# Kernel optimization log

Hardware: AMD Instinct MI355X
Metric: run time of the kernel (lower is better)

Reference implementation:

```python
import jax, jax.numpy as jnp
import numpy as np

TWO_PI = 6.283185307179586
B, D, NC = 2097152, 8, 1024


def _apply_rot(s0, s1, phi, theta, omega):
    """Apply PennyLane Rot(phi, theta, omega) = RZ(omega) RY(theta) RZ(phi)
    to a batch of single-qubit states (s0, s1). All angle args float32."""
    c = jnp.cos(theta * 0.5)
    s = jnp.sin(theta * 0.5)
    u00 = jnp.exp(-0.5j * (phi + omega)) * c
    u01 = -jnp.exp(0.5j * (phi - omega)) * s
    u10 = jnp.exp(-0.5j * (phi - omega)) * s
    u11 = jnp.exp(0.5j * (phi + omega)) * c
    return u00 * s0 + u01 * s1, u10 * s0 + u11 * s1


def setup_inputs() -> dict:
    key = jax.random.key(0)
    k1, k2, k3 = jax.random.split(key, 3)
    instance = jax.random.uniform(k1, (B, D, 3), dtype=jnp.float32) * TWO_PI
    concept_index = jax.random.randint(k2, (B, D), 0, NC, dtype=jnp.int64)
    # product concept -> init uniform in [0, 2*pi)
    concept_weights = jax.random.uniform(k3, (NC, 3), dtype=jnp.float32) * TWO_PI
    return {"instance": instance, "concept_index": concept_index,
            "concept_weights": concept_weights}


def reference(instance, concept_index, concept_weights):
    # embedding gather: [B, D, 3]
    concept = concept_weights[concept_index]
    # per-domain single-qubit circuit: |0> -> Rot(instance) -> Rot(concept)
    s0 = jnp.ones((B, D), dtype=jnp.complex64)
    s1 = jnp.zeros((B, D), dtype=jnp.complex64)
    s0, s1 = _apply_rot(s0, s1, instance[..., 0], instance[..., 1], instance[..., 2])
    s0, s1 = _apply_rot(s0, s1, concept[..., 0], concept[..., 1], concept[..., 2])
    # expval(PauliZ) per wire, then map to probability as in forward()
    z = (s0.real * s0.real + s0.imag * s0.imag) - (s1.real * s1.real + s1.imag * s1.imag)
    return z * 0.5 + 0.5  # [batch, domain]
```

## Files before the change

kernel.cpp:

```cpp
#include <hip/hip_runtime.h>
#include <math.h>

#define NCONCEPT 1024


__global__ __launch_bounds__(256) void vqc_kernel(
    const float* __restrict__ inst,
    const int*   __restrict__ idx,
    const float* __restrict__ w,
    float*       __restrict__ out,
    int n)
{
    __shared__ float4 tab[NCONCEPT];

    for (int c = threadIdx.x; c < NCONCEPT; c += blockDim.x) {
        float ph2 = w[c * 3 + 0];
        float th2 = w[c * 3 + 1];
        float sth2, cth2, sph2, cph2;
        __sincosf(th2, &sth2, &cth2);
        __sincosf(ph2, &sph2, &cph2);
        tab[c] = make_float4(cth2, sth2, cph2, sph2);
    }
    __syncthreads();

    const int tid    = blockIdx.x * blockDim.x + threadIdx.x;
    const int stride = gridDim.x * blockDim.x;
    const int nquads = n >> 2;

    const float4* __restrict__ inst4 = (const float4*)inst;
    const int4*   __restrict__ idx4  = (const int4*)idx;
    float4*       __restrict__ out4  = (float4*)out;

    for (int q = tid; q < nquads; q += stride) {
        float4 a = inst4[q * 3 + 0];
        float4 b = inst4[q * 3 + 1];
        float4 c = inst4[q * 3 + 2];
        int4   ix = idx4[q];

        float th[4] = { a.y, b.x, b.w, c.z };
        float om[4] = { a.z, b.y, c.x, c.w };
        int   id[4] = { ix.x, ix.y, ix.z, ix.w };

        float res[4];
        #pragma unroll
        for (int e = 0; e < 4; ++e) {
            float4 t = tab[id[e]];
            float s1, c1, so, co;
            __sincosf(th[e], &s1, &c1);
            __sincosf(om[e], &so, &co);
            float cop = co * t.z - so * t.w;
            float z   = t.x * c1 - t.y * s1 * cop;
            res[e] = fmaf(z, 0.5f, 0.5f);
        }
        out4[q] = make_float4(res[0], res[1], res[2], res[3]);
    }

    for (int i = (nquads << 2) + tid; i < n; i += stride) {
        float th1 = inst[i * 3 + 1];
        float om1 = inst[i * 3 + 2];
        float4 t = tab[idx[i]];
        float s1, c1, so, co;
        __sincosf(th1, &s1, &c1);
        __sincosf(om1, &so, &co);
        float cop = co * t.z - so * t.w;
        float z   = t.x * c1 - t.y * s1 * cop;
        out[i] = fmaf(z, 0.5f, 0.5f);
    }
}

extern "C" void kernel_launch(void* const* d_in, const int* in_sizes, int n_in,
                              void* d_out, int out_size, void* d_ws, size_t ws_size,
                              hipStream_t stream) {
    const float* inst = (const float*)d_in[0];
    const int*   idx  = (const int*)d_in[1];
    const float* w    = (const float*)d_in[2];
    float*       out  = (float*)d_out;

    const int n = in_sizes[1];
    const int blocks = 2048;
    vqc_kernel<<<blocks, 256, 0, stream>>>(inst, idx, w, out, n);
}
```

Baseline: 64.54 us.

## Process eight elements per thread with nontemporal loads and a split LUT

Each thread now handles eight elements per iteration, issuing six 16-byte instance loads and two index loads, all nontemporal, plus nontemporal output stores. The shared concept table is split into a cos array and a premultiplied (sin*cos, sin*sin) float2 array. This removes per-element multiplies and shrinks LDS reads from 16 to 12 bytes. The larger unroll adds more loads in flight per thread but raises register pressure.

```diff
diff --git a/kernel.cpp b/kernel.cpp
--- a/kernel.cpp
+++ b/kernel.cpp
@@ -2,6 +2,10 @@
 #include <math.h>
 
 #define NCONCEPT 1024
+
+typedef float fx4 __attribute__((ext_vector_type(4)));
+typedef int   ix4 __attribute__((ext_vector_type(4)));
+typedef float fx2 __attribute__((ext_vector_type(2)));
 
 
 __global__ __launch_bounds__(256) void vqc_kernel(
@@ -11,7 +15,8 @@
     float*       __restrict__ out,
     int n)
 {
-    __shared__ float4 tab[NCONCEPT];
+    __shared__ float tabA[NCONCEPT];
+    __shared__ fx2   tabB[NCONCEPT];
 
     for (int c = threadIdx.x; c < NCONCEPT; c += blockDim.x) {
         float ph2 = w[c * 3 + 0];
@@ -19,51 +24,62 @@
         float sth2, cth2, sph2, cph2;
         __sincosf(th2, &sth2, &cth2);
         __sincosf(ph2, &sph2, &cph2);
-        tab[c] = make_float4(cth2, sth2, cph2, sph2);
+        tabA[c] = cth2;
+        fx2 b; b.x = sth2 * cph2; b.y = sth2 * sph2;
+        tabB[c] = b;
     }
     __syncthreads();
 
     const int tid    = blockIdx.x * blockDim.x + threadIdx.x;
     const int stride = gridDim.x * blockDim.x;
-    const int nquads = n >> 2;
+    const int nocts  = n >> 3;
 
-    const float4* __restrict__ inst4 = (const float4*)inst;
-    const int4*   __restrict__ idx4  = (const int4*)idx;
-    float4*       __restrict__ out4  = (float4*)out;
+    const fx4* __restrict__ inst4 = (const fx4*)inst;
+    const ix4* __restrict__ idx4  = (const ix4*)idx;
+    fx4*       __restrict__ out4  = (fx4*)out;
 
-    for (int q = tid; q < nquads; q += stride) {
-        float4 a = inst4[q * 3 + 0];
-        float4 b = inst4[q * 3 + 1];
-        float4 c = inst4[q * 3 + 2];
-        int4   ix = idx4[q];
+    for (int q = tid; q < nocts; q += stride) {
+        fx4 a0 = __builtin_nontemporal_load(&inst4[q * 6 + 0]);
+        fx4 a1 = __builtin_nontemporal_load(&inst4[q * 6 + 1]);
+        fx4 a2 = __builtin_nontemporal_load(&inst4[q * 6 + 2]);
+        fx4 a3 = __builtin_nontemporal_load(&inst4[q * 6 + 3]);
+        fx4 a4 = __builtin_nontemporal_load(&inst4[q * 6 + 4]);
+        fx4 a5 = __builtin_nontemporal_load(&inst4[q * 6 + 5]);
+        ix4 i0 = __builtin_nontemporal_load(&idx4[q * 2 + 0]);
+        ix4 i1 = __builtin_nontemporal_load(&idx4[q * 2 + 1]);
 
-        float th[4] = { a.y, b.x, b.w, c.z };
-        float om[4] = { a.z, b.y, c.x, c.w };
-        int   id[4] = { ix.x, ix.y, ix.z, ix.w };
+        float th[8] = { a0.y, a1.x, a1.w, a2.z, a3.y, a4.x, a4.w, a5.z };
+        float om[8] = { a0.z, a1.y, a2.x, a2.w, a3.z, a4.y, a5.x, a5.w };
+        int   id[8] = { i0.x, i0.y, i0.z, i0.w, i1.x, i1.y, i1.z, i1.w };
 
-        float res[4];
+        float res[8];
         #pragma unroll
-        for (int e = 0; e < 4; ++e) {
-            float4 t = tab[id[e]];
+        for (int e = 0; e < 8; ++e) {
+            float A  = tabA[id[e]];
+            fx2   Bv = tabB[id[e]];
             float s1, c1, so, co;
             __sincosf(th[e], &s1, &c1);
             __sincosf(om[e], &so, &co);
-            float cop = co * t.z - so * t.w;
-            float z   = t.x * c1 - t.y * s1 * cop;
+            float cop = Bv.x * co - Bv.y * so;
+            float z   = A * c1 - s1 * cop;
             res[e] = fmaf(z, 0.5f, 0.5f);
         }
-        out4[q] = make_float4(res[0], res[1], res[2], res[3]);
+        fx4 r0, r1;
+        r0.x = res[0]; r0.y = res[1]; r0.z = res[2]; r0.w = res[3];
+        r1.x = res[4]; r1.y = res[5]; r1.z = res[6]; r1.w = res[7];
+        __builtin_nontemporal_store(r0, &out4[q * 2 + 0]);
+        __builtin_nontemporal_store(r1, &out4[q * 2 + 1]);
     }
 
-    for (int i = (nquads << 2) + tid; i < n; i += stride) {
+    for (int i = (nocts << 3) + tid; i < n; i += stride) {
         float th1 = inst[i * 3 + 1];
         float om1 = inst[i * 3 + 2];
-        float4 t = tab[idx[i]];
+        float A   = tabA[idx[i]];
+        fx2   Bv  = tabB[idx[i]];
         float s1, c1, so, co;
         __sincosf(th1, &s1, &c1);
         __sincosf(om1, &so, &co);
-        float cop = co * t.z - so * t.w;
-        float z   = t.x * c1 - t.y * s1 * cop;
+        float z = A * c1 - s1 * (Bv.x * co - Bv.y * so);
         out[i] = fmaf(z, 0.5f, 0.5f);
     }
 }
```

Result: slower. 111.9 us (+73.3%).

## Switch to per-element strided loads with 4-way unrolled batching and prefolded table

Applied to the files above, without the earlier changes.

Replaces the per-thread quad processing, which used three float4 instance loads and one int4 index load, with per-element accesses. Each thread now issues four independent element loads across grid strides, reading only theta and omega as an unaligned float2, so the unused phi is never requested. The concept table now stores cos(theta), sin(theta)cos(phi) and sin(theta)sin(phi) precomputed, saving a multiply per element. The cost is narrower, stride-3 gathers in place of wide vector loads, which may reduce coalescing efficiency, though cache lines are still fully fetched.

```diff
diff --git a/kernel.cpp b/kernel.cpp
--- a/kernel.cpp
+++ b/kernel.cpp
@@ -2,68 +2,65 @@
 #include <math.h>
 
 #define NCONCEPT 1024
+#define TPB 256
+#define UNROLL 4
+
+typedef float fx4  __attribute__((ext_vector_type(4)));
+typedef float fx2u __attribute__((ext_vector_type(2), aligned(4)));
 
 
-__global__ __launch_bounds__(256) void vqc_kernel(
+__global__ __launch_bounds__(TPB) void vqc_kernel(
     const float* __restrict__ inst,
     const int*   __restrict__ idx,
     const float* __restrict__ w,
     float*       __restrict__ out,
     int n)
 {
-    __shared__ float4 tab[NCONCEPT];
+    __shared__ fx4 tab[NCONCEPT];
 
-    for (int c = threadIdx.x; c < NCONCEPT; c += blockDim.x) {
+    for (int c = threadIdx.x; c < NCONCEPT; c += TPB) {
         float ph2 = w[c * 3 + 0];
         float th2 = w[c * 3 + 1];
         float sth2, cth2, sph2, cph2;
         __sincosf(th2, &sth2, &cth2);
         __sincosf(ph2, &sph2, &cph2);
-        tab[c] = make_float4(cth2, sth2, cph2, sph2);
+        fx4 t; t.x = cth2; t.y = sth2 * cph2; t.z = sth2 * sph2; t.w = 0.0f;
+        tab[c] = t;
     }
     __syncthreads();
 
-    const int tid    = blockIdx.x * blockDim.x + threadIdx.x;
-    const int stride = gridDim.x * blockDim.x;
-    const int nquads = n >> 2;
+    const int tid = blockIdx.x * TPB + threadIdx.x;
+    const int T   = gridDim.x * TPB;
 
-    const float4* __restrict__ inst4 = (const float4*)inst;
-    const int4*   __restrict__ idx4  = (const int4*)idx;
-    float4*       __restrict__ out4  = (float4*)out;
-
-    for (int q = tid; q < nquads; q += stride) {
-        float4 a = inst4[q * 3 + 0];
-        float4 b = inst4[q * 3 + 1];
-        float4 c = inst4[q * 3 + 2];
-        int4   ix = idx4[q];
-
-        float th[4] = { a.y, b.x, b.w, c.z };
-        float om[4] = { a.z, b.y, c.x, c.w };
-        int   id[4] = { ix.x, ix.y, ix.z, ix.w };
-
-        float res[4];
+    int i = tid;
+    for (; i + (UNROLL - 1) * T < n; i += UNROLL * T) {
+        fx2u to_[UNROLL];
+        int  id_[UNROLL];
         #pragma unroll
-        for (int e = 0; e < 4; ++e) {
-            float4 t = tab[id[e]];
+        for (int u = 0; u < UNROLL; ++u) {
+            const int e = i + u * T;
+            to_[u] = *(const fx2u*)(inst + (size_t)e * 3 + 1);
+            id_[u] = idx[e];
+        }
+        #pragma unroll
+        for (int u = 0; u < UNROLL; ++u) {
+            const int e = i + u * T;
+            fx4 t4 = tab[id_[u]];
             float s1, c1, so, co;
-            __sincosf(th[e], &s1, &c1);
-            __sincosf(om[e], &so, &co);
-            float cop = co * t.z - so * t.w;
-            float z   = t.x * c1 - t.y * s1 * cop;
-            res[e] = fmaf(z, 0.5f, 0.5f);
+            __sincosf(to_[u].x, &s1, &c1);
+            __sincosf(to_[u].y, &so, &co);
+            float z = t4.x * c1 - s1 * (t4.y * co - t4.z * so);
+            out[e] = fmaf(z, 0.5f, 0.5f);
         }
-        out4[q] = make_float4(res[0], res[1], res[2], res[3]);
     }
-
-    for (int i = (nquads << 2) + tid; i < n; i += stride) {
-        float th1 = inst[i * 3 + 1];
-        float om1 = inst[i * 3 + 2];
-        float4 t = tab[idx[i]];
+    for (; i < n; i += T) {
+        float th1 = inst[(size_t)i * 3 + 1];
+        float om1 = inst[(size_t)i * 3 + 2];
+        fx4 t4 = tab[idx[i]];
         float s1, c1, so, co;
         __sincosf(th1, &s1, &c1);
         __sincosf(om1, &so, &co);
-        float cop = co * t.z - so * t.w;
-        float z   = t.x * c1 - t.y * s1 * cop;
+        float z = t4.x * c1 - s1 * (t4.y * co - t4.z * so);
         out[i] = fmaf(z, 0.5f, 0.5f);
     }
 }
@@ -77,6 +74,5 @@
     float*       out  = (float*)d_out;
 
     const int n = in_sizes[1];
-    const int blocks = 2048;
-    vqc_kernel<<<blocks, 256, 0, stream>>>(inst, idx, w, out, n);
+    vqc_kernel<<<2048, TPB, 0, stream>>>(inst, idx, w, out, n);
 }
```

Result: slower. 66.69 us (+3.3%).
